# Performance work log

Hardware: AMD Instinct MI355X
Metric: run time of the kernel (lower is better)

## Reference

```python
import jax, jax.numpy as jnp
import numpy as np

N_NODES = 8192
N_FEAT = 256
N_EDGES = 131072
K = 4


def setup_inputs() -> dict:
    key = jax.random.key(0)
    k1, k2, k3 = jax.random.split(key, 3)
    x = jax.random.normal(k1, (N_NODES, N_FEAT), dtype=jnp.float32)
    edge_index = jax.random.randint(k2, (2, N_EDGES), 0, N_NODES, dtype=jnp.int64)
    edge_weight = jax.random.uniform(k3, (N_EDGES,), dtype=jnp.float32)
    return {"k": K, "x": x, "edge_index": edge_index, "edge_weight": edge_weight}


def reference(k, x, edge_index, edge_weight):
    n = x.shape[0]
    src, dst = edge_index[0], edge_index[1]
    # Symmetrized dense adjacency, matching the torch loop:
    #   adj[src, dst] = w  then  adj[dst, src] += w
    adj = jnp.zeros((n, n), dtype=x.dtype)
    adj = adj.at[src, dst].set(edge_weight)
    adj = adj.at[dst, src].add(edge_weight)
    # M = [I | A | A^2 | ... | A^{k-1}] (N x kN) times block_diag(x,...,x)
    # (kN x kF) is exactly concat([A^j @ x for j in 0..k-1], axis=1) -- we
    # compute that directly and never form the block-diagonal zeros.
    outs = [x]
    h = x
    for _ in range(1, k):
        h = adj @ h  # A^j @ x  (A symmetric, so order is immaterial)
        outs.append(h)
    return jnp.concatenate(outs, axis=1)  # [N, k*F]
```

## Files before the change

kernel.cpp:

```cpp
#include <hip/hip_runtime.h>

#define N_NODES 8192
#define N_FEAT  256
#define N_EDGES 131072
#define KPOW    4
#define OUT_LD  1024
#define RCAP    128
#define COL_MASK 8191u

static __device__ __forceinline__ float bflo(unsigned u) {
    union { unsigned i; float f; } v; v.i = u << 16; return v.f;
}
static __device__ __forceinline__ float bfhi(unsigned u) {
    union { unsigned i; float f; } v; v.i = u & 0xffff0000u; return v.f;
}
static __device__ __forceinline__ unsigned short f2bf(float f) {
    union { float f; unsigned i; } v = { f };
    return (unsigned short)((v.i + 0x7fffu + ((v.i >> 16) & 1u)) >> 16);
}

__global__ void k_scatter_copy(const int* __restrict__ ei, const float* __restrict__ ew,
                               int* __restrict__ len, uint2* __restrict__ ent,
                               const float* __restrict__ x, float* __restrict__ out,
                               unsigned short* __restrict__ xb) {
    if (blockIdx.x < 2048) {
        int t = blockIdx.x * blockDim.x + threadIdx.x;
        int row = t >> 6;
        int lane = t & 63;
        float4 v = *(const float4*)(x + (size_t)row * N_FEAT + lane * 4);
        *(float4*)(out + (size_t)row * OUT_LD + lane * 4) = v;
        ushort4 b;
        b.x = f2bf(v.x); b.y = f2bf(v.y); b.z = f2bf(v.z); b.w = f2bf(v.w);
        *(ushort4*)(xb + (size_t)row * N_FEAT + lane * 4) = b;
    } else {
        int e = (blockIdx.x - 2048) * blockDim.x + threadIdx.x;
        if (e >= N_EDGES) return;
        int src = ei[e];
        int dst = ei[N_EDGES + e];
        unsigned wbits = __float_as_uint(ew[e]);
        int s0 = atomicAdd(&len[dst], 1);
        if (s0 < RCAP) ent[(size_t)dst * RCAP + s0] = make_uint2((unsigned)src, wbits);
        int s1 = atomicAdd(&len[src], 1);
        if (s1 < RCAP) ent[(size_t)src * RCAP + s1] =
            make_uint2((1u << 30) | ((unsigned)e << 13) | (unsigned)dst, wbits);
    }
}

__global__ __launch_bounds__(256) void k_dedup(uint2* __restrict__ ent) {
    int lane = threadIdx.x & 63;
    int row = blockIdx.x * 4 + (threadIdx.x >> 6);
    size_t base = (size_t)row * RCAP;
    unsigned v0 = ent[base + lane].x;
    unsigned v1 = ent[base + 64 + lane].x;
    bool k0 = false, k1 = false;
    for (int j = 0; j < 64; ++j) {
        unsigned b = (unsigned)__shfl((int)v0, j);
        if (b >> 30) {
            k0 |= (((b ^ v0) & COL_MASK) == 0u) && (b > v0);
            k1 |= (((b ^ v1) & COL_MASK) == 0u) && (b > v1);
        }
        unsigned b2 = (unsigned)__shfl((int)v1, j);
        if (b2 >> 30) {
            k0 |= (((b2 ^ v0) & COL_MASK) == 0u) && (b2 > v0);
            k1 |= (((b2 ^ v1) & COL_MASK) == 0u) && (b2 > v1);
        }
    }
    if (k0 && (v0 >> 30)) ent[base + lane].y = 0u;
    if (k1 && (v1 >> 30)) ent[base + 64 + lane].y = 0u;
}

__global__ __launch_bounds__(256) void k_spmm(const int* __restrict__ len,
                                              const uint2* __restrict__ ent,
                                              const unsigned short* __restrict__ hinb,
                                              float* __restrict__ hout,
                                              unsigned short* __restrict__ houtb,
                                              int write_bf) {
    int lane = threadIdx.x & 63;
    int row = __builtin_amdgcn_readfirstlane(blockIdx.x * 4 + (threadIdx.x >> 6));
    int n = len[row];
    if (n > RCAP) n = RCAP;
    const uint4* e4 = (const uint4*)(ent + (size_t)row * RCAP);
    float ax = 0.f, ay = 0.f, az = 0.f, aw = 0.f;
    int ng = (n + 7) >> 3;

    uint4 q0, q1, q2, q3;
    if (ng > 0) { q0 = e4[0]; q1 = e4[1]; q2 = e4[2]; q3 = e4[3]; }
    for (int g = 0; g < ng; ++g) {
        int gp = (g + 1 < 16) ? (g + 1) : 0;
        uint4 p0 = e4[gp * 4 + 0], p1 = e4[gp * 4 + 1],
              p2 = e4[gp * 4 + 2], p3 = e4[gp * 4 + 3];
        uint4 qq[4] = { q0, q1, q2, q3 };
#pragma unroll
        for (int k = 0; k < 4; ++k) {
            unsigned ca = qq[k].x & COL_MASK; float wa = __uint_as_float(qq[k].y);
            unsigned cb = qq[k].z & COL_MASK; float wb = __uint_as_float(qq[k].w);
            uint2 ua = *(const uint2*)(hinb + (size_t)ca * N_FEAT + lane * 4);
            uint2 ub = *(const uint2*)(hinb + (size_t)cb * N_FEAT + lane * 4);
            ax += wa * bflo(ua.x); ay += wa * bfhi(ua.x);
            az += wa * bflo(ua.y); aw += wa * bfhi(ua.y);
            ax += wb * bflo(ub.x); ay += wb * bfhi(ub.x);
            az += wb * bflo(ub.y); aw += wb * bfhi(ub.y);
        }
        q0 = p0; q1 = p1; q2 = p2; q3 = p3;
    }

    *(float4*)(hout + (size_t)row * OUT_LD + lane * 4) =
        make_float4(ax, ay, az, aw);
    if (write_bf) {
        ushort4 b;
        b.x = f2bf(ax); b.y = f2bf(ay); b.z = f2bf(az); b.w = f2bf(aw);
        *(ushort4*)(houtb + (size_t)row * N_FEAT + lane * 4) = b;
    }
}

extern "C" void kernel_launch(void* const* d_in, const int* in_sizes, int n_in,
                              void* d_out, int out_size, void* d_ws, size_t ws_size,
                              hipStream_t stream) {
    const float* x  = (const float*)d_in[1];
    const int*   ei = (const int*)d_in[2];
    const float* ew = (const float*)d_in[3];
    float* out = (float*)d_out;

    int* len   = (int*)d_ws;
    uint2* ent = (uint2*)(len + N_NODES);
    unsigned short* hb0 = (unsigned short*)(ent + (size_t)N_NODES * RCAP);
    unsigned short* hb1 = hb0 + (size_t)N_NODES * N_FEAT;
    unsigned short* hb2 = hb1 + (size_t)N_NODES * N_FEAT;

    hipMemsetAsync(d_ws, 0, (size_t)N_NODES * sizeof(int)
                            + (size_t)N_NODES * RCAP * sizeof(uint2), stream);

    const int TB = 256;
    const int EB = N_EDGES / TB;

    k_scatter_copy<<<2048 + EB, TB, 0, stream>>>(ei, ew, len, ent, x, out, hb0);
    k_dedup<<<N_NODES / 4, TB, 0, stream>>>(ent);

    const unsigned short* hin = hb0;
    for (int j = 1; j < KPOW; ++j) {
        float* hout = out + (size_t)j * N_FEAT;
        unsigned short* houtb = (j == 1) ? hb1 : hb2;
        int write_bf = (j < KPOW - 1) ? 1 : 0;
        k_spmm<<<N_NODES / 4, TB, 0, stream>>>(len, ent, hin, hout, houtb, write_bf);
        hin = houtb;
    }
}
```

Measured before the change: 145.7 us.

## Skip memset of adjacency entries, pad rows in dedup, use nontemporal access

Stops zeroing the whole 8 MB entry table on every call. Only the row lengths are cleared, and the dedup kernel now zeroes the weights of the padding slots up to the next group of eight, so the SpMM tail reads contribute nothing. Dedup loops only over the valid entry count instead of all 128 slots. Nontemporal loads and stores are added across the kernels to reduce cache pollution. The risk is that stale entries beyond the padded group are still prefetched by SpMM, though they are never used.

Measured after the change: 146.3 us. About the same (+0.4%).

```diff
diff --git a/kernel.cpp b/kernel.cpp
--- a/kernel.cpp
+++ b/kernel.cpp
@@ -7,6 +7,10 @@
 #define OUT_LD  1024
 #define RCAP    128
 #define COL_MASK 8191u
+
+typedef float    f32x4 __attribute__((ext_vector_type(4)));
+typedef unsigned u32x4 __attribute__((ext_vector_type(4)));
+typedef unsigned u32x2 __attribute__((ext_vector_type(2)));
 
 static __device__ __forceinline__ float bflo(unsigned u) {
     union { unsigned i; float f; } v; v.i = u << 16; return v.f;
@@ -20,57 +24,73 @@
 }
 
 __global__ void k_scatter_copy(const int* __restrict__ ei, const float* __restrict__ ew,
-                               int* __restrict__ len, uint2* __restrict__ ent,
+                               int* __restrict__ len, u32x2* __restrict__ ent,
                                const float* __restrict__ x, float* __restrict__ out,
                                unsigned short* __restrict__ xb) {
     if (blockIdx.x < 2048) {
         int t = blockIdx.x * blockDim.x + threadIdx.x;
         int row = t >> 6;
         int lane = t & 63;
-        float4 v = *(const float4*)(x + (size_t)row * N_FEAT + lane * 4);
-        *(float4*)(out + (size_t)row * OUT_LD + lane * 4) = v;
+        f32x4 v = __builtin_nontemporal_load(
+            (const f32x4*)(x + (size_t)row * N_FEAT + lane * 4));
+        __builtin_nontemporal_store(v, (f32x4*)(out + (size_t)row * OUT_LD + lane * 4));
         ushort4 b;
         b.x = f2bf(v.x); b.y = f2bf(v.y); b.z = f2bf(v.z); b.w = f2bf(v.w);
         *(ushort4*)(xb + (size_t)row * N_FEAT + lane * 4) = b;
     } else {
         int e = (blockIdx.x - 2048) * blockDim.x + threadIdx.x;
         if (e >= N_EDGES) return;
-        int src = ei[e];
-        int dst = ei[N_EDGES + e];
-        unsigned wbits = __float_as_uint(ew[e]);
+        int src = __builtin_nontemporal_load(ei + e);
+        int dst = __builtin_nontemporal_load(ei + N_EDGES + e);
+        unsigned wbits = __float_as_uint(__builtin_nontemporal_load(ew + e));
         int s0 = atomicAdd(&len[dst], 1);
-        if (s0 < RCAP) ent[(size_t)dst * RCAP + s0] = make_uint2((unsigned)src, wbits);
+        if (s0 < RCAP) {
+            u32x2 v; v.x = (unsigned)src; v.y = wbits;
+            __builtin_nontemporal_store(v, ent + (size_t)dst * RCAP + s0);
+        }
         int s1 = atomicAdd(&len[src], 1);
-        if (s1 < RCAP) ent[(size_t)src * RCAP + s1] =
-            make_uint2((1u << 30) | ((unsigned)e << 13) | (unsigned)dst, wbits);
+        if (s1 < RCAP) {
+            u32x2 v; v.x = (1u << 30) | ((unsigned)e << 13) | (unsigned)dst; v.y = wbits;
+            __builtin_nontemporal_store(v, ent + (size_t)src * RCAP + s1);
+        }
     }
 }
 
-__global__ __launch_bounds__(256) void k_dedup(uint2* __restrict__ ent) {
+__global__ __launch_bounds__(256) void k_dedup(const int* __restrict__ len,
+                                               unsigned* __restrict__ entw) {
     int lane = threadIdx.x & 63;
     int row = blockIdx.x * 4 + (threadIdx.x >> 6);
+    int n = __builtin_amdgcn_readfirstlane(len[row]);
+    if (n > RCAP) n = RCAP;
     size_t base = (size_t)row * RCAP;
-    unsigned v0 = ent[base + lane].x;
-    unsigned v1 = ent[base + 64 + lane].x;
+    unsigned v0 = __builtin_nontemporal_load(entw + 2 * (base + lane));
+    unsigned v1 = __builtin_nontemporal_load(entw + 2 * (base + 64 + lane));
     bool k0 = false, k1 = false;
-    for (int j = 0; j < 64; ++j) {
+    int j0 = n < 64 ? n : 64;
+    for (int j = 0; j < j0; ++j) {
         unsigned b = (unsigned)__shfl((int)v0, j);
         if (b >> 30) {
             k0 |= (((b ^ v0) & COL_MASK) == 0u) && (b > v0);
             k1 |= (((b ^ v1) & COL_MASK) == 0u) && (b > v1);
         }
-        unsigned b2 = (unsigned)__shfl((int)v1, j);
-        if (b2 >> 30) {
-            k0 |= (((b2 ^ v0) & COL_MASK) == 0u) && (b2 > v0);
-            k1 |= (((b2 ^ v1) & COL_MASK) == 0u) && (b2 > v1);
+    }
+    for (int j = 0; j < n - 64; ++j) {
+        unsigned b = (unsigned)__shfl((int)v1, j);
+        if (b >> 30) {
+            k0 |= (((b ^ v0) & COL_MASK) == 0u) && (b > v0);
+            k1 |= (((b ^ v1) & COL_MASK) == 0u) && (b > v1);
         }
     }
-    if (k0 && (v0 >> 30)) ent[base + lane].y = 0u;
-    if (k1 && (v1 >> 30)) ent[base + 64 + lane].y = 0u;
+    int ngs = 8 * ((n + 7) >> 3);
+    int s1 = 64 + lane;
+    if (lane < n) { if (k0 && (v0 >> 30)) entw[2 * (base + lane) + 1] = 0u; }
+    else if (lane < ngs) entw[2 * (base + lane) + 1] = 0u;
+    if (s1 < n) { if (k1 && (v1 >> 30)) entw[2 * (base + s1) + 1] = 0u; }
+    else if (s1 < ngs) entw[2 * (base + s1) + 1] = 0u;
 }
 
 __global__ __launch_bounds__(256) void k_spmm(const int* __restrict__ len,
-                                              const uint2* __restrict__ ent,
+                                              const u32x2* __restrict__ ent,
                                               const unsigned short* __restrict__ hinb,
                                               float* __restrict__ hout,
                                               unsigned short* __restrict__ houtb,
@@ -79,17 +99,24 @@
     int row = __builtin_amdgcn_readfirstlane(blockIdx.x * 4 + (threadIdx.x >> 6));
     int n = len[row];
     if (n > RCAP) n = RCAP;
-    const uint4* e4 = (const uint4*)(ent + (size_t)row * RCAP);
+    const u32x4* e4 = (const u32x4*)(ent + (size_t)row * RCAP);
     float ax = 0.f, ay = 0.f, az = 0.f, aw = 0.f;
     int ng = (n + 7) >> 3;
 
-    uint4 q0, q1, q2, q3;
-    if (ng > 0) { q0 = e4[0]; q1 = e4[1]; q2 = e4[2]; q3 = e4[3]; }
+    u32x4 q0, q1, q2, q3;
+    if (ng > 0) {
+        q0 = __builtin_nontemporal_load(e4 + 0);
+        q1 = __builtin_nontemporal_load(e4 + 1);
+        q2 = __builtin_nontemporal_load(e4 + 2);
+        q3 = __builtin_nontemporal_load(e4 + 3);
+    }
     for (int g = 0; g < ng; ++g) {
         int gp = (g + 1 < 16) ? (g + 1) : 0;
-        uint4 p0 = e4[gp * 4 + 0], p1 = e4[gp * 4 + 1],
-              p2 = e4[gp * 4 + 2], p3 = e4[gp * 4 + 3];
-        uint4 qq[4] = { q0, q1, q2, q3 };
+        u32x4 p0 = __builtin_nontemporal_load(e4 + gp * 4 + 0);
+        u32x4 p1 = __builtin_nontemporal_load(e4 + gp * 4 + 1);
+        u32x4 p2 = __builtin_nontemporal_load(e4 + gp * 4 + 2);
+        u32x4 p3 = __builtin_nontemporal_load(e4 + gp * 4 + 3);
+        u32x4 qq[4] = { q0, q1, q2, q3 };
 #pragma unroll
         for (int k = 0; k < 4; ++k) {
             unsigned ca = qq[k].x & COL_MASK; float wa = __uint_as_float(qq[k].y);
@@ -104,8 +131,8 @@
         q0 = p0; q1 = p1; q2 = p2; q3 = p3;
     }
 
-    *(float4*)(hout + (size_t)row * OUT_LD + lane * 4) =
-        make_float4(ax, ay, az, aw);
+    f32x4 r; r.x = ax; r.y = ay; r.z = az; r.w = aw;
+    __builtin_nontemporal_store(r, (f32x4*)(hout + (size_t)row * OUT_LD + lane * 4));
     if (write_bf) {
         ushort4 b;
         b.x = f2bf(ax); b.y = f2bf(ay); b.z = f2bf(az); b.w = f2bf(aw);
@@ -122,19 +149,18 @@
     float* out = (float*)d_out;
 
     int* len   = (int*)d_ws;
-    uint2* ent = (uint2*)(len + N_NODES);
+    u32x2* ent = (u32x2*)(len + N_NODES);
     unsigned short* hb0 = (unsigned short*)(ent + (size_t)N_NODES * RCAP);
     unsigned short* hb1 = hb0 + (size_t)N_NODES * N_FEAT;
     unsigned short* hb2 = hb1 + (size_t)N_NODES * N_FEAT;
 
-    hipMemsetAsync(d_ws, 0, (size_t)N_NODES * sizeof(int)
-                            + (size_t)N_NODES * RCAP * sizeof(uint2), stream);
+    (void)hipMemsetAsync(len, 0, (size_t)N_NODES * sizeof(int), stream);
 
     const int TB = 256;
     const int EB = N_EDGES / TB;
 
     k_scatter_copy<<<2048 + EB, TB, 0, stream>>>(ei, ew, len, ent, x, out, hb0);
-    k_dedup<<<N_NODES / 4, TB, 0, stream>>>(ent);
+    k_dedup<<<N_NODES / 4, TB, 0, stream>>>(len, (unsigned*)ent);
 
     const unsigned short* hin = hb0;
     for (int j = 1; j < KPOW; ++j) {
```
